# Kernel optimization log

Measured on AMD Instinct MI355X. Metric: run time of the kernel, lower is better.

Reference implementation:

```python
import jax, jax.numpy as jnp
import numpy as np

N_NODES = 50000
N_EDGES = 500000
N_FEAT = 128
EMB_DIM = 1024
HIDDEN = 128
OUT_DIM = 10
VOCAB = 55049
N_GRAPHS = 64


def setup_inputs() -> dict:
    key = jax.random.key(0)
    ks = jax.random.split(key, 12)
    x = jax.random.normal(ks[0], (N_NODES, N_FEAT), dtype=jnp.float32)
    edge_weight = jax.random.uniform(ks[1], (N_EDGES,), dtype=jnp.float32)
    edge_index = jax.random.randint(ks[2], (2, N_EDGES), 0, N_NODES)
    batch = jnp.sort(jax.random.randint(ks[3], (N_NODES,), 0, N_GRAPHS))
    node_ids = jax.random.randint(ks[4], (N_NODES,), 0, VOCAB)
    emb_table = jax.random.normal(ks[5], (VOCAB, EMB_DIM), dtype=jnp.float32)
    d_in = N_FEAT + EMB_DIM
    W1 = jax.random.normal(ks[6], (d_in, HIDDEN), dtype=jnp.float32) / np.sqrt(d_in)
    b1 = jnp.zeros((HIDDEN,), dtype=jnp.float32)
    W2 = jax.random.normal(ks[7], (HIDDEN, HIDDEN), dtype=jnp.float32) / np.sqrt(HIDDEN)
    b2 = jnp.zeros((HIDDEN,), dtype=jnp.float32)
    fcW = jax.random.normal(ks[8], (HIDDEN, OUT_DIM), dtype=jnp.float32) / np.sqrt(HIDDEN)
    fcb = jnp.zeros((OUT_DIM,), dtype=jnp.float32)
    return dict(x=x, edge_weight=edge_weight, emb_table=emb_table, W1=W1, b1=b1,
                W2=W2, b2=b2, fcW=fcW, fcb=fcb,
                edge_index=edge_index, batch=batch, node_ids=node_ids)


def gcn_conv(x, edge_index, edge_weight, W, b, n_nodes):
    # PyG GCNConv: x' = D^{-1/2} (A + I) D^{-1/2} (x W) + b, self-loop weight = 1
    x = x @ W
    src, dst = edge_index[0], edge_index[1]
    loop = jnp.arange(n_nodes)
    src = jnp.concatenate([src, loop])
    dst = jnp.concatenate([dst, loop])
    ew = jnp.concatenate([edge_weight, jnp.ones((n_nodes,), x.dtype)])
    deg = jax.ops.segment_sum(ew, dst, num_segments=n_nodes)
    dinv = jnp.where(deg > 0, jax.lax.rsqrt(deg), 0.0)
    norm = dinv[src] * ew * dinv[dst]  # [E+N]
    msgs = norm[:, None] * x[src]      # [E+N, H] gather
    out = jax.ops.segment_sum(msgs, dst, num_segments=n_nodes)  # scatter-add
    return out + b


def reference(x, edge_weight, emb_table, W1, b1, W2, b2, fcW, fcb,
              edge_index, batch, node_ids):
    n = x.shape[0]
    h = jnp.concatenate([x, emb_table[node_ids]], axis=1)  # [N, F+E]
    h = jax.nn.relu(gcn_conv(h, edge_index, edge_weight, W1, b1, n))
    h = jax.nn.relu(gcn_conv(h, edge_index, edge_weight, W2, b2, n))
    # global mean pool per graph (dropout is identity in eval)
    sums = jax.ops.segment_sum(h, batch, num_segments=N_GRAPHS)
    counts = jax.ops.segment_sum(jnp.ones((n,), h.dtype), batch, num_segments=N_GRAPHS)
    pooled = sums / jnp.maximum(counts, 1.0)[:, None]
    return pooled @ fcW + fcb
```

## Files before the change

### kernel.cpp

```cpp
#include <hip/hip_runtime.h>
#include <hip/hip_bf16.h>

#define N_NODES 50000
#define N_EDGES 500000
#define N_FEAT 128
#define EMB_DIM 1024
#define HIDDEN 128
#define OUT_DIM 10
#define N_GRAPHS 64
#define NB_NODE 196

typedef __attribute__((ext_vector_type(8))) short short8;
typedef __attribute__((ext_vector_type(4))) float f32x4;

__device__ __forceinline__ unsigned short f2bf(float f) {
    unsigned int u = __float_as_uint(f);
    return (unsigned short)((u + 0x7fffu + ((u >> 16) & 1u)) >> 16);
}
__device__ __forceinline__ float bflo(unsigned int r) { return __uint_as_float(r << 16); }
__device__ __forceinline__ float bfhi(unsigned int r) { return __uint_as_float(r & 0xffff0000u); }
__device__ __forceinline__ unsigned int packbf(float lo, float hi) {
    return ((unsigned int)f2bf(hi) << 16) | f2bf(lo);
}

__global__ __launch_bounds__(256) void k_init(unsigned long long* __restrict__ dc,
                                              float* __restrict__ sums,
                                              float* __restrict__ counts) {
    int i = blockIdx.x * 256 + threadIdx.x;
    if (i < N_NODES) dc[i] = 0ULL;
    if (i < N_GRAPHS * HIDDEN) sums[i] = 0.0f;
    if (i < N_GRAPHS) counts[i] = 0.0f;
}

__global__ __launch_bounds__(256) void k_deg(const int* __restrict__ dst,
                                             const float* __restrict__ ew,
                                             unsigned long long* __restrict__ dc) {
    int e = blockIdx.x * 256 + threadIdx.x;
    if (e < N_EDGES) {
        unsigned int fx = (unsigned int)(ew[e] * 16777216.0f);
        atomicAdd(&dc[dst[e]], (1ULL << 32) | (unsigned long long)fx);
    }
}

__global__ __launch_bounds__(256) void k_scan1(const unsigned long long* __restrict__ dc,
                                               int* __restrict__ bsum) {
    __shared__ int wsum[4];
    int i = blockIdx.x * 256 + threadIdx.x;
    int v = (i < N_NODES) ? (int)((const uint2*)dc)[i].y : 0;
#pragma unroll
    for (int off = 32; off; off >>= 1) v += __shfl_down(v, off, 64);
    if ((threadIdx.x & 63) == 0) wsum[threadIdx.x >> 6] = v;
    __syncthreads();
    if (threadIdx.x == 0) bsum[blockIdx.x] = wsum[0] + wsum[1] + wsum[2] + wsum[3];
}

__global__ __launch_bounds__(256) void k_scan2(int* __restrict__ bsum) {
    __shared__ int sh[256];
    int t = threadIdx.x;
    int v = (t < NB_NODE) ? bsum[t] : 0;
    sh[t] = v;
    __syncthreads();
    for (int off = 1; off < 256; off <<= 1) {
        int add = (t >= off) ? sh[t - off] : 0;
        __syncthreads();
        sh[t] += add;
        __syncthreads();
    }
    if (t < NB_NODE) bsum[t] = sh[t] - v;
}

__global__ __launch_bounds__(256) void k_scan3(const unsigned long long* __restrict__ dc,
                                               const int* __restrict__ bofs,
                                               int* __restrict__ cursor,
                                               int* __restrict__ rowptr,
                                               float* __restrict__ dinv) {
    __shared__ int sh[256];
    const int t = threadIdx.x;
    const int i = blockIdx.x * 256 + t;
    uint2 d = (i < N_NODES) ? ((const uint2*)dc)[i] : make_uint2(0u, 0u);
    int v = (int)d.y;
    sh[t] = v;
    __syncthreads();
    for (int off = 1; off < 256; off <<= 1) {
        int add = (t >= off) ? sh[t - off] : 0;
        __syncthreads();
        sh[t] += add;
        __syncthreads();
    }
    int ex = sh[t] - v + bofs[blockIdx.x];
    if (i < N_NODES) {
        rowptr[i] = ex;
        cursor[i] = ex;
        float deg = 1.0f + (float)d.x * (1.0f / 16777216.0f);
        dinv[i] = 1.0f / sqrtf(deg);
    }
    if (i == 0) rowptr[N_NODES] = N_EDGES;
}

__global__ __launch_bounds__(256) void k_fill(const int* __restrict__ src,
                                              const int* __restrict__ dst,
                                              const float* __restrict__ ew,
                                              const float* __restrict__ dinv,
                                              int* __restrict__ cursor,
                                              int2* __restrict__ csr) {
    int e = blockIdx.x * 256 + threadIdx.x;
    if (e >= N_EDGES) return;
    int s = src[e], d = dst[e];
    int pos = atomicAdd(&cursor[d], 1);
    float norm = dinv[s] * ew[e] * dinv[d];
    csr[pos] = make_int2(s, __float_as_int(norm));
}

__device__ __forceinline__ void prep_one(const float* __restrict__ W,
                                         unsigned short* __restrict__ Wt,
                                         int K, int t) {
    int n = t & 127;
    int c = t >> 7;
    if (c * 16 >= K) return;
    short8 h0, h1;
#pragma unroll
    for (int i = 0; i < 16; i++) {
        unsigned short h = f2bf(W[(size_t)(c * 16 + i) * HIDDEN + n]);
        if (i < 8) h0[i] = (short)h;
        else       h1[i - 8] = (short)h;
    }
    size_t o = (size_t)n * K + c * 16;
    *(short8*)&Wt[o] = h0;
    *(short8*)&Wt[o + 8] = h1;
}

__global__ __launch_bounds__(256) void k_prep(const float* __restrict__ W1,
                                              unsigned short* __restrict__ Wt1,
                                              const float* __restrict__ W2,
                                              unsigned short* __restrict__ Wt2) {
    int b = blockIdx.x;
    if (b < 36) prep_one(W1, Wt1, N_FEAT + EMB_DIM, b * 256 + threadIdx.x);
    else        prep_one(W2, Wt2, HIDDEN, (b - 36) * 256 + threadIdx.x);
}

template <int MODE>
__global__ __launch_bounds__(256) void k_gemm(const float* __restrict__ X,
                                              const unsigned short* __restrict__ Xb,
                                              const float* __restrict__ EMB,
                                              const int* __restrict__ ids,
                                              const unsigned short* __restrict__ Wt,
                                              unsigned short* __restrict__ tbf, int K) {
    __shared__ unsigned short As[128][40];
    __shared__ unsigned short Bs[128][40];

    const int tid = threadIdx.x;
    const int lane = tid & 63;
    const int wv = tid >> 6;
    const int wm = wv >> 1, wn = wv & 1;
    const int fr = lane & 15;
    const int fq = lane >> 4;
    const int mBase = blockIdx.x * 128;

    const int aRow = tid >> 1;
    const int aOff = (tid & 1) * 16;
    const int m = mBase + aRow;
    const int mc = (m < N_NODES) ? m : (N_NODES - 1);
    int embRow = 0;
    if (MODE == 0) embRow = ids[mc];

    f32x4 acc[4][4];
#pragma unroll
    for (int i = 0; i < 4; i++)
#pragma unroll
        for (int j = 0; j < 4; j++) acc[i][j] = (f32x4){0.f, 0.f, 0.f, 0.f};

    float av[16];
    short8 axb0, axb1;
    short8 bh0, bh1;
    {
        if (MODE == 0) {
            const float* aptr = X + (size_t)mc * N_FEAT + aOff;
            *(float4*)&av[0]  = *(const float4*)(aptr);
            *(float4*)&av[4]  = *(const float4*)(aptr + 4);
            *(float4*)&av[8]  = *(const float4*)(aptr + 8);
            *(float4*)&av[12] = *(const float4*)(aptr + 12);
        } else {
            const unsigned short* aptr = Xb + (size_t)mc * HIDDEN + aOff;
            axb0 = *(const short8*)(aptr);
            axb1 = *(const short8*)(aptr + 8);
        }
        size_t bo = (size_t)aRow * K + aOff;
        bh0 = *(const short8*)&Wt[bo];
        bh1 = *(const short8*)&Wt[bo + 8];
    }

    for (int k0 = 0; k0 < K; k0 += 32) {
        short8 ah0, ah1;
        if (MODE == 0) {
#pragma unroll
            for (int i = 0; i < 16; i++) {
                unsigned short h = f2bf(av[i]);
                if (i < 8) ah0[i] = (short)h;
                else       ah1[i - 8] = (short)h;
            }
        } else {
            ah0 = axb0; ah1 = axb1;
        }
        *(short8*)&As[aRow][aOff] = ah0; *(short8*)&As[aRow][aOff + 8] = ah1;
        *(short8*)&Bs[aRow][aOff] = bh0; *(short8*)&Bs[aRow][aOff + 8] = bh1;
        __syncthreads();

        int k1 = k0 + 32;
        if (k1 < K) {
            if (MODE == 0) {
                const float* aptr = (k1 < N_FEAT)
                    ? X + (size_t)mc * N_FEAT + k1 + aOff
                    : EMB + (size_t)embRow * EMB_DIM + (k1 - N_FEAT) + aOff;
                *(float4*)&av[0]  = *(const float4*)(aptr);
                *(float4*)&av[4]  = *(const float4*)(aptr + 4);
                *(float4*)&av[8]  = *(const float4*)(aptr + 8);
                *(float4*)&av[12] = *(const float4*)(aptr + 12);
            } else {
                const unsigned short* aptr = Xb + (size_t)mc * HIDDEN + k1 + aOff;
                axb0 = *(const short8*)(aptr);
                axb1 = *(const short8*)(aptr + 8);
            }
            size_t bo = (size_t)aRow * K + k1 + aOff;
            bh0 = *(const short8*)&Wt[bo];
            bh1 = *(const short8*)&Wt[bo + 8];
        }

        short8 aF[4], bF[4];
#pragma unroll
        for (int i = 0; i < 4; i++) {
            aF[i] = *(const short8*)&As[wm * 64 + i * 16 + fr][fq * 8];
            bF[i] = *(const short8*)&Bs[wn * 64 + i * 16 + fr][fq * 8];
        }

#pragma unroll
        for (int i = 0; i < 4; i++)
#pragma unroll
            for (int j = 0; j < 4; j++)
                acc[i][j] = __builtin_amdgcn_mfma_f32_16x16x32_bf16(aF[i], bF[j], acc[i][j], 0, 0, 0);
        __syncthreads();
    }

#pragma unroll
    for (int i = 0; i < 4; i++) {
#pragma unroll
        for (int j = 0; j < 4; j++) {
            int gcol = wn * 64 + j * 16 + fr;
#pragma unroll
            for (int r = 0; r < 4; r++) {
                int grow = mBase + wm * 64 + i * 16 + fq * 4 + r;
                if (grow < N_NODES) tbf[(size_t)grow * HIDDEN + gcol] = f2bf(acc[i][j][r]);
            }
        }
    }
}

template <int POOL, int NWAVE>
__global__ __launch_bounds__(NWAVE * 64) void k_agg(const int2* __restrict__ csr,
                                                    const int* __restrict__ rowptr,
                                                    const float* __restrict__ dinv,
                                                    const unsigned short* __restrict__ tbf,
                                                    const float* __restrict__ bias,
                                                    const int* __restrict__ batch,
                                                    unsigned short* __restrict__ outb,
                                                    float* __restrict__ sums,
                                                    float* __restrict__ counts) {
    __shared__ float lsum[HIDDEN];
    __shared__ int lcnt;
    const int wv = threadIdx.x >> 6;
    const int lane = threadIdx.x & 63;
    const int grp = lane >> 4;
    const int q = lane & 15;
    const int n = blockIdx.x * NWAVE + wv;
    const uint4* t128 = (const uint4*)tbf;

    if (POOL) {
        if (threadIdx.x < HIDDEN) lsum[threadIdx.x] = 0.f;
        if (threadIdx.x == 0) lcnt = 0;
        __syncthreads();
    }

    float acc[8] = {};
    if (n < N_NODES) {
        const int beg = rowptr[n];
        const int end = rowptr[n + 1];
        const float di = dinv[n];
        const float wself = (grp == 0) ? di * di : 0.f;
        uint4 sr = t128[(size_t)n * 16 + q];
        acc[0] = wself * bflo(sr.x); acc[1] = wself * bfhi(sr.x);
        acc[2] = wself * bflo(sr.y); acc[3] = wself * bfhi(sr.y);
        acc[4] = wself * bflo(sr.z); acc[5] = wself * bfhi(sr.z);
        acc[6] = wself * bflo(sr.w); acc[7] = wself * bfhi(sr.w);
        if (grp == 0) {
            float4 b0 = ((const float4*)bias)[q * 2];
            float4 b1 = ((const float4*)bias)[q * 2 + 1];
            acc[0] += b0.x; acc[1] += b0.y; acc[2] += b0.z; acc[3] += b0.w;
            acc[4] += b1.x; acc[5] += b1.y; acc[6] += b1.z; acc[7] += b1.w;
        }

        for (int base = beg; base < end; base += 64) {
            int cnt = end - base; if (cnt > 64) cnt = 64;
            int2 ce = (lane < cnt) ? csr[base + lane] : make_int2(0, 0);
            int j = 0;
            for (; j + 8 <= cnt; j += 8) {
                int   sA = __shfl(ce.x, j + grp);
                float wA = __int_as_float(__shfl(ce.y, j + grp));
                int   sB = __shfl(ce.x, j + 4 + grp);
                float wB = __int_as_float(__shfl(ce.y, j + 4 + grp));
                uint4 rA = t128[(size_t)sA * 16 + q];
                uint4 rB = t128[(size_t)sB * 16 + q];
                acc[0] = fmaf(wA, bflo(rA.x), acc[0]); acc[1] = fmaf(wA, bfhi(rA.x), acc[1]);
                acc[2] = fmaf(wA, bflo(rA.y), acc[2]); acc[3] = fmaf(wA, bfhi(rA.y), acc[3]);
                acc[4] = fmaf(wA, bflo(rA.z), acc[4]); acc[5] = fmaf(wA, bfhi(rA.z), acc[5]);
                acc[6] = fmaf(wA, bflo(rA.w), acc[6]); acc[7] = fmaf(wA, bfhi(rA.w), acc[7]);
                acc[0] = fmaf(wB, bflo(rB.x), acc[0]); acc[1] = fmaf(wB, bfhi(rB.x), acc[1]);
                acc[2] = fmaf(wB, bflo(rB.y), acc[2]); acc[3] = fmaf(wB, bfhi(rB.y), acc[3]);
                acc[4] = fmaf(wB, bflo(rB.z), acc[4]); acc[5] = fmaf(wB, bfhi(rB.z), acc[5]);
                acc[6] = fmaf(wB, bflo(rB.w), acc[6]); acc[7] = fmaf(wB, bfhi(rB.w), acc[7]);
            }
            for (; j < cnt; j += 4) {
                int   s = __shfl(ce.x, j + grp);
                float w = __int_as_float(__shfl(ce.y, j + grp));
                uint4 r = t128[(size_t)s * 16 + q];
                acc[0] = fmaf(w, bflo(r.x), acc[0]); acc[1] = fmaf(w, bfhi(r.x), acc[1]);
                acc[2] = fmaf(w, bflo(r.y), acc[2]); acc[3] = fmaf(w, bfhi(r.y), acc[3]);
                acc[4] = fmaf(w, bflo(r.z), acc[4]); acc[5] = fmaf(w, bfhi(r.z), acc[5]);
                acc[6] = fmaf(w, bflo(r.w), acc[6]); acc[7] = fmaf(w, bfhi(r.w), acc[7]);
            }
        }
    }

#pragma unroll
    for (int i = 0; i < 8; i++) {
        acc[i] += __shfl_xor(acc[i], 16);
        acc[i] += __shfl_xor(acc[i], 32);
    }

    if (!POOL) {
        if (n < N_NODES && grp == 0) {
#pragma unroll
            for (int i = 0; i < 8; i++) acc[i] = fmaxf(acc[i], 0.f);
            uint4 o;
            o.x = packbf(acc[0], acc[1]);
            o.y = packbf(acc[2], acc[3]);
            o.z = packbf(acc[4], acc[5]);
            o.w = packbf(acc[6], acc[7]);
            ((uint4*)outb)[(size_t)n * 16 + q] = o;
        }
    } else {
        if (n < N_NODES && grp == 0) {
#pragma unroll
            for (int i = 0; i < 8; i++) acc[i] = fmaxf(acc[i], 0.f);
            int g = batch[n];
            int g0 = batch[blockIdx.x * NWAVE];
            if (g == g0) {
#pragma unroll
                for (int i = 0; i < 8; i++) atomicAdd(&lsum[q * 8 + i], acc[i]);
                if (lane == 0) atomicAdd(&lcnt, 1);
            } else {
#pragma unroll
                for (int i = 0; i < 8; i++) atomicAdd(&sums[g * HIDDEN + q * 8 + i], acc[i]);
                if (lane == 0) atomicAdd(&counts[g], 1.0f);
            }
        }
        __syncthreads();
        int g0 = batch[blockIdx.x * NWAVE];
        if (threadIdx.x < HIDDEN) atomicAdd(&sums[g0 * HIDDEN + threadIdx.x], lsum[threadIdx.x]);
        if (threadIdx.x == 0) atomicAdd(&counts[g0], (float)lcnt);
    }
}

__global__ __launch_bounds__(64) void k_final(const float* __restrict__ sums,
                                              const float* __restrict__ counts,
                                              const float* __restrict__ fcW,
                                              const float* __restrict__ fcb,
                                              float* __restrict__ out) {
    int g = blockIdx.x;
    int o = threadIdx.x;
    if (o >= OUT_DIM) return;
    float inv = 1.0f / fmaxf(counts[g], 1.0f);
    float acc = 0.f;
    for (int f = 0; f < HIDDEN; f++)
        acc = fmaf(sums[g * HIDDEN + f], fcW[f * OUT_DIM + o], acc);
    out[g * OUT_DIM + o] = acc * inv + fcb[o];
}

extern "C" void kernel_launch(void* const* d_in, const int* in_sizes, int n_in,
                              void* d_out, int out_size, void* d_ws, size_t ws_size,
                              hipStream_t stream) {
    const float* x      = (const float*)d_in[0];
    const float* ew     = (const float*)d_in[1];
    const float* emb    = (const float*)d_in[2];
    const float* W1     = (const float*)d_in[3];
    const float* b1     = (const float*)d_in[4];
    const float* W2     = (const float*)d_in[5];
    const float* b2     = (const float*)d_in[6];
    const float* fcW    = (const float*)d_in[7];
    const float* fcb    = (const float*)d_in[8];
    const int* edge_idx = (const int*)d_in[9];
    const int* batch    = (const int*)d_in[10];
    const int* node_ids = (const int*)d_in[11];
    float* out = (float*)d_out;

    const int* src = edge_idx;
    const int* dst = edge_idx + N_EDGES;

    float* ws     = (float*)d_ws;
    float* dinv   = ws;
    unsigned long long* dc = (unsigned long long*)(ws + 50048);
    int*   cursor = (int*)(ws + 150048);
    int*   rowptr = (int*)(ws + 200096);
    int*   bsum   = (int*)(ws + 250152);
    int2*  csr    = (int2*)(ws + 250408);
    unsigned short* tbf   = (unsigned short*)(ws + 1250408);
    unsigned short* out1b = (unsigned short*)(ws + 4450408);
    float* sums   = ws + 7650408;
    float* counts = sums + N_GRAPHS * HIDDEN;
    unsigned short* wt1 = (unsigned short*)(ws + 7658664);
    unsigned short* wt2 = (unsigned short*)(ws + 7732392);

    const int NB_EDGE = (N_EDGES + 255) / 256;
    const int NB_GEMM = (N_NODES + 127) / 128;
    const int K1 = N_FEAT + EMB_DIM;

    k_init <<<NB_NODE, 256, 0, stream>>>(dc, sums, counts);
    k_deg  <<<NB_EDGE, 256, 0, stream>>>(dst, ew, dc);
    k_scan1<<<NB_NODE, 256, 0, stream>>>(dc, bsum);
    k_scan2<<<1, 256, 0, stream>>>(bsum);
    k_scan3<<<NB_NODE, 256, 0, stream>>>(dc, bsum, cursor, rowptr, dinv);
    k_fill <<<NB_EDGE, 256, 0, stream>>>(src, dst, ew, dinv, cursor, csr);
    k_prep <<<40, 256, 0, stream>>>(W1, wt1, W2, wt2);

    k_gemm<0><<<NB_GEMM, 256, 0, stream>>>(x, nullptr, emb, node_ids, wt1, tbf, K1);
    k_agg<0, 4><<<(N_NODES + 3) / 4, 256, 0, stream>>>(csr, rowptr, dinv, tbf, b1,
                                                       batch, out1b, sums, counts);

    k_gemm<1><<<NB_GEMM, 256, 0, stream>>>(nullptr, out1b, nullptr, nullptr, wt2, tbf, HIDDEN);
    k_agg<1, 16><<<(N_NODES + 15) / 16, 1024, 0, stream>>>(csr, rowptr, dinv, tbf, b2,
                                                           batch, nullptr, sums, counts);

    k_final<<<N_GRAPHS, 64, 0, stream>>>(sums, counts, fcW, fcb, out);
}
```

Measured before the change: 522.8 us.

## Fuse prep/scan launches, vectorize edge kernels, shrink GEMM tile, one node per quarter-wave

Folds the weight-prep kernel into the init kernel and merges the single-block scan into scan3, which cuts two launches. The edge degree and fill kernels now process four edges per thread using vector loads. The GEMM M-tile shrinks from 128 to 64 rows so more blocks are launched. The aggregation kernels give each 16-lane group its own node instead of splitting one node's edges across the wave, which removes the cross-group shuffle reduction but can leave lanes idle on nodes with uneven degree. Each scan3 block now redoes the full block-offset scan.

After: 548.8 us. 5.0% more time.

```diff
diff --git a/kernel.cpp b/kernel.cpp
--- a/kernel.cpp
+++ b/kernel.cpp
@@ -23,22 +23,55 @@
     return ((unsigned int)f2bf(hi) << 16) | f2bf(lo);
 }
 
+__device__ __forceinline__ void prep_one(const float* __restrict__ W,
+                                         unsigned short* __restrict__ Wt,
+                                         int K, int t) {
+    int n = t & 127;
+    int c = t >> 7;
+    if (c * 16 >= K) return;
+    short8 h0, h1;
+#pragma unroll
+    for (int i = 0; i < 16; i++) {
+        unsigned short h = f2bf(W[(size_t)(c * 16 + i) * HIDDEN + n]);
+        if (i < 8) h0[i] = (short)h;
+        else       h1[i - 8] = (short)h;
+    }
+    size_t o = (size_t)n * K + c * 16;
+    *(short8*)&Wt[o] = h0;
+    *(short8*)&Wt[o + 8] = h1;
+}
+
 __global__ __launch_bounds__(256) void k_init(unsigned long long* __restrict__ dc,
                                               float* __restrict__ sums,
-                                              float* __restrict__ counts) {
-    int i = blockIdx.x * 256 + threadIdx.x;
-    if (i < N_NODES) dc[i] = 0ULL;
-    if (i < N_GRAPHS * HIDDEN) sums[i] = 0.0f;
-    if (i < N_GRAPHS) counts[i] = 0.0f;
+                                              float* __restrict__ counts,
+                                              const float* __restrict__ W1,
+                                              unsigned short* __restrict__ Wt1,
+                                              const float* __restrict__ W2,
+                                              unsigned short* __restrict__ Wt2) {
+    int b = blockIdx.x;
+    if (b < NB_NODE) {
+        int i = b * 256 + threadIdx.x;
+        if (i < N_NODES) dc[i] = 0ULL;
+        if (i < N_GRAPHS * HIDDEN) sums[i] = 0.0f;
+        if (i < N_GRAPHS) counts[i] = 0.0f;
+    } else if (b < NB_NODE + 36) {
+        prep_one(W1, Wt1, N_FEAT + EMB_DIM, (b - NB_NODE) * 256 + threadIdx.x);
+    } else {
+        prep_one(W2, Wt2, HIDDEN, (b - NB_NODE - 36) * 256 + threadIdx.x);
+    }
 }
 
 __global__ __launch_bounds__(256) void k_deg(const int* __restrict__ dst,
                                              const float* __restrict__ ew,
                                              unsigned long long* __restrict__ dc) {
-    int e = blockIdx.x * 256 + threadIdx.x;
-    if (e < N_EDGES) {
-        unsigned int fx = (unsigned int)(ew[e] * 16777216.0f);
-        atomicAdd(&dc[dst[e]], (1ULL << 32) | (unsigned long long)fx);
+    int e4 = blockIdx.x * 256 + threadIdx.x;
+    if (e4 < N_EDGES / 4) {
+        int4 d4 = ((const int4*)dst)[e4];
+        float4 w4 = ((const float4*)ew)[e4];
+        atomicAdd(&dc[d4.x], (1ULL << 32) | (unsigned long long)(unsigned int)(w4.x * 16777216.0f));
+        atomicAdd(&dc[d4.y], (1ULL << 32) | (unsigned long long)(unsigned int)(w4.y * 16777216.0f));
+        atomicAdd(&dc[d4.z], (1ULL << 32) | (unsigned long long)(unsigned int)(w4.z * 16777216.0f));
+        atomicAdd(&dc[d4.w], (1ULL << 32) | (unsigned long long)(unsigned int)(w4.w * 16777216.0f));
     }
 }
 
@@ -54,28 +87,27 @@
     if (threadIdx.x == 0) bsum[blockIdx.x] = wsum[0] + wsum[1] + wsum[2] + wsum[3];
 }
 
-__global__ __launch_bounds__(256) void k_scan2(int* __restrict__ bsum) {
-    __shared__ int sh[256];
-    int t = threadIdx.x;
-    int v = (t < NB_NODE) ? bsum[t] : 0;
-    sh[t] = v;
-    __syncthreads();
-    for (int off = 1; off < 256; off <<= 1) {
-        int add = (t >= off) ? sh[t - off] : 0;
-        __syncthreads();
-        sh[t] += add;
-        __syncthreads();
-    }
-    if (t < NB_NODE) bsum[t] = sh[t] - v;
-}
-
 __global__ __launch_bounds__(256) void k_scan3(const unsigned long long* __restrict__ dc,
-                                               const int* __restrict__ bofs,
+                                               const int* __restrict__ bsum,
                                                int* __restrict__ cursor,
                                                int* __restrict__ rowptr,
                                                float* __restrict__ dinv) {
+    __shared__ int sb[256];
     __shared__ int sh[256];
+    __shared__ int bofs_s;
     const int t = threadIdx.x;
+
+    int vb = (t < NB_NODE) ? bsum[t] : 0;
+    sb[t] = vb;
+    __syncthreads();
+    for (int off = 1; off < 256; off <<= 1) {
+        int add = (t >= off) ? sb[t - off] : 0;
+        __syncthreads();
+        sb[t] += add;
+        __syncthreads();
+    }
+    if (t == blockIdx.x) bofs_s = sb[t] - vb;
+
     const int i = blockIdx.x * 256 + t;
     uint2 d = (i < N_NODES) ? ((const uint2*)dc)[i] : make_uint2(0u, 0u);
     int v = (int)d.y;
@@ -87,7 +119,7 @@
         sh[t] += add;
         __syncthreads();
     }
-    int ex = sh[t] - v + bofs[blockIdx.x];
+    int ex = sh[t] - v + bofs_s;
     if (i < N_NODES) {
         rowptr[i] = ex;
         cursor[i] = ex;
@@ -103,39 +135,27 @@
                                               const float* __restrict__ dinv,
                                               int* __restrict__ cursor,
                                               int2* __restrict__ csr) {
-    int e = blockIdx.x * 256 + threadIdx.x;
-    if (e >= N_EDGES) return;
-    int s = src[e], d = dst[e];
-    int pos = atomicAdd(&cursor[d], 1);
-    float norm = dinv[s] * ew[e] * dinv[d];
-    csr[pos] = make_int2(s, __float_as_int(norm));
-}
-
-__device__ __forceinline__ void prep_one(const float* __restrict__ W,
-                                         unsigned short* __restrict__ Wt,
-                                         int K, int t) {
-    int n = t & 127;
-    int c = t >> 7;
-    if (c * 16 >= K) return;
-    short8 h0, h1;
-#pragma unroll
-    for (int i = 0; i < 16; i++) {
-        unsigned short h = f2bf(W[(size_t)(c * 16 + i) * HIDDEN + n]);
-        if (i < 8) h0[i] = (short)h;
-        else       h1[i - 8] = (short)h;
-    }
-    size_t o = (size_t)n * K + c * 16;
-    *(short8*)&Wt[o] = h0;
-    *(short8*)&Wt[o + 8] = h1;
-}
-
-__global__ __launch_bounds__(256) void k_prep(const float* __restrict__ W1,
-                                              unsigned short* __restrict__ Wt1,
-                                              const float* __restrict__ W2,
-                                              unsigned short* __restrict__ Wt2) {
-    int b = blockIdx.x;
-    if (b < 36) prep_one(W1, Wt1, N_FEAT + EMB_DIM, b * 256 + threadIdx.x);
-    else        prep_one(W2, Wt2, HIDDEN, (b - 36) * 256 + threadIdx.x);
+    int e4 = blockIdx.x * 256 + threadIdx.x;
+    if (e4 >= N_EDGES / 4) return;
+    int4 s4 = ((const int4*)src)[e4];
+    int4 d4 = ((const int4*)dst)[e4];
+    float4 w4 = ((const float4*)ew)[e4];
+    {
+        int pos = atomicAdd(&cursor[d4.x], 1);
+        csr[pos] = make_int2(s4.x, __float_as_int(dinv[s4.x] * w4.x * dinv[d4.x]));
+    }
+    {
+        int pos = atomicAdd(&cursor[d4.y], 1);
+        csr[pos] = make_int2(s4.y, __float_as_int(dinv[s4.y] * w4.y * dinv[d4.y]));
+    }
+    {
+        int pos = atomicAdd(&cursor[d4.z], 1);
+        csr[pos] = make_int2(s4.z, __float_as_int(dinv[s4.z] * w4.z * dinv[d4.z]));
+    }
+    {
+        int pos = atomicAdd(&cursor[d4.w], 1);
+        csr[pos] = make_int2(s4.w, __float_as_int(dinv[s4.w] * w4.w * dinv[d4.w]));
+    }
 }
 
 template <int MODE>
@@ -145,7 +165,7 @@
                                               const int* __restrict__ ids,
                                               const unsigned short* __restrict__ Wt,
                                               unsigned short* __restrict__ tbf, int K) {
-    __shared__ unsigned short As[128][40];
+    __shared__ unsigned short As[64][40];
     __shared__ unsigned short Bs[128][40];
 
     const int tid = threadIdx.x;
@@ -154,55 +174,51 @@
     const int wm = wv >> 1, wn = wv & 1;
     const int fr = lane & 15;
     const int fq = lane >> 4;
-    const int mBase = blockIdx.x * 128;
-
-    const int aRow = tid >> 1;
-    const int aOff = (tid & 1) * 16;
+    const int mBase = blockIdx.x * 64;
+
+    const int aRow = tid >> 2;
+    const int aOff = (tid & 3) * 8;
+    const int bCol = tid >> 1;
+    const int bOff = (tid & 1) * 16;
+
     const int m = mBase + aRow;
     const int mc = (m < N_NODES) ? m : (N_NODES - 1);
     int embRow = 0;
     if (MODE == 0) embRow = ids[mc];
 
-    f32x4 acc[4][4];
-#pragma unroll
-    for (int i = 0; i < 4; i++)
+    f32x4 acc[2][4];
+#pragma unroll
+    for (int i = 0; i < 2; i++)
 #pragma unroll
         for (int j = 0; j < 4; j++) acc[i][j] = (f32x4){0.f, 0.f, 0.f, 0.f};
 
-    float av[16];
-    short8 axb0, axb1;
+    float av[8];
+    short8 axb;
     short8 bh0, bh1;
     {
         if (MODE == 0) {
             const float* aptr = X + (size_t)mc * N_FEAT + aOff;
-            *(float4*)&av[0]  = *(const float4*)(aptr);
-            *(float4*)&av[4]  = *(const float4*)(aptr + 4);
-            *(float4*)&av[8]  = *(const float4*)(aptr + 8);
-            *(float4*)&av[12] = *(const float4*)(aptr + 12);
+            *(float4*)&av[0] = *(const float4*)(aptr);
+            *(float4*)&av[4] = *(const float4*)(aptr + 4);
         } else {
-            const unsigned short* aptr = Xb + (size_t)mc * HIDDEN + aOff;
-            axb0 = *(const short8*)(aptr);
-            axb1 = *(const short8*)(aptr + 8);
-        }
-        size_t bo = (size_t)aRow * K + aOff;
+            axb = *(const short8*)(Xb + (size_t)mc * HIDDEN + aOff);
+        }
+        size_t bo = (size_t)bCol * K + bOff;
         bh0 = *(const short8*)&Wt[bo];
         bh1 = *(const short8*)&Wt[bo + 8];
     }
 
     for (int k0 = 0; k0 < K; k0 += 32) {
-        short8 ah0, ah1;
+        short8 ah;
         if (MODE == 0) {
 #pragma unroll
-            for (int i = 0; i < 16; i++) {
-                unsigned short h = f2bf(av[i]);
-                if (i < 8) ah0[i] = (short)h;
-                else       ah1[i - 8] = (short)h;
-            }
+            for (int i = 0; i < 8; i++) ah[i] = (short)f2bf(av[i]);
         } else {
-            ah0 = axb0; ah1 = axb1;
-        }
-        *(short8*)&As[aRow][aOff] = ah0; *(short8*)&As[aRow][aOff + 8] = ah1;
-        *(short8*)&Bs[aRow][aOff] = bh0; *(short8*)&Bs[aRow][aOff + 8] = bh1;
+            ah = axb;
+        }
+        *(short8*)&As[aRow][aOff] = ah;
+        *(short8*)&Bs[bCol][bOff] = bh0;
+        *(short8*)&Bs[bCol][bOff + 8] = bh1;
         __syncthreads();
 
         int k1 = k0 + 32;
@@ -211,29 +227,26 @@
                 const float* aptr = (k1 < N_FEAT)
                     ? X + (size_t)mc * N_FEAT + k1 + aOff
                     : EMB + (size_t)embRow * EMB_DIM + (k1 - N_FEAT) + aOff;
-                *(float4*)&av[0]  = *(const float4*)(aptr);
-                *(float4*)&av[4]  = *(const float4*)(aptr + 4);
-                *(float4*)&av[8]  = *(const float4*)(aptr + 8);
-                *(float4*)&av[12] = *(const float4*)(aptr + 12);
+                *(float4*)&av[0] = *(const float4*)(aptr);
+                *(float4*)&av[4] = *(const float4*)(aptr + 4);
             } else {
-                const unsigned short* aptr = Xb + (size_t)mc * HIDDEN + k1 + aOff;
-                axb0 = *(const short8*)(aptr);
-                axb1 = *(const short8*)(aptr + 8);
+                axb = *(const short8*)(Xb + (size_t)mc * HIDDEN + k1 + aOff);
             }
-            size_t bo = (size_t)aRow * K + k1 + aOff;
+            size_t bo = (size_t)bCol * K + k1 + bOff;
             bh0 = *(const short8*)&Wt[bo];
             bh1 = *(const short8*)&Wt[bo + 8];
         }
 
-        short8 aF[4], bF[4];
-#pragma unroll
-        for (int i = 0; i < 4; i++) {
-            aF[i] = *(const short8*)&As[wm * 64 + i * 16 + fr][fq * 8];
-            bF[i] = *(const short8*)&Bs[wn * 64 + i * 16 + fr][fq * 8];
-        }
-
-#pragma unroll
-        for (int i = 0; i < 4; i++)
+        short8 aF[2], bF[4];
+#pragma unroll
+        for (int i = 0; i < 2; i++)
+            aF[i] = *(const short8*)&As[wm * 32 + i * 16 + fr][fq * 8];
+#pragma unroll
+        for (int j = 0; j < 4; j++)
+            bF[j] = *(const short8*)&Bs[wn * 64 + j * 16 + fr][fq * 8];
+
+#pragma unroll
+        for (int i = 0; i < 2; i++)
 #pragma unroll
             for (int j = 0; j < 4; j++)
                 acc[i][j] = __builtin_amdgcn_mfma_f32_16x16x32_bf16(aF[i], bF[j], acc[i][j], 0, 0, 0);
@@ -241,13 +254,13 @@
     }
 
 #pragma unroll
-    for (int i = 0; i < 4; i++) {
+    for (int i = 0; i < 2; i++) {
 #pragma unroll
         for (int j = 0; j < 4; j++) {
             int gcol = wn * 64 + j * 16 + fr;
 #pragma unroll
             for (int r = 0; r < 4; r++) {
-                int grow = mBase + wm * 64 + i * 16 + fq * 4 + r;
+                int grow = mBase + wm * 32 + i * 16 + fq * 4 + r;
                 if (grow < N_NODES) tbf[(size_t)grow * HIDDEN + gcol] = f2bf(acc[i][j][r]);
             }
         }
@@ -268,9 +281,9 @@
     __shared__ int lcnt;
     const int wv = threadIdx.x >> 6;
     const int lane = threadIdx.x & 63;
-    const int grp = lane >> 4;
+    const int g = lane >> 4;
     const int q = lane & 15;
-    const int n = blockIdx.x * NWAVE + wv;
+    const int n = (blockIdx.x * NWAVE + wv) * 4 + g;
     const uint4* t128 = (const uint4*)tbf;
 
     if (POOL) {
@@ -284,61 +297,55 @@
         const int beg = rowptr[n];
         const int end = rowptr[n + 1];
         const float di = dinv[n];
-        const float wself = (grp == 0) ? di * di : 0.f;
+        const float wself = di * di;
         uint4 sr = t128[(size_t)n * 16 + q];
-        acc[0] = wself * bflo(sr.x); acc[1] = wself * bfhi(sr.x);
-        acc[2] = wself * bflo(sr.y); acc[3] = wself * bfhi(sr.y);
-        acc[4] = wself * bflo(sr.z); acc[5] = wself * bfhi(sr.z);
-        acc[6] = wself * bflo(sr.w); acc[7] = wself * bfhi(sr.w);
-        if (grp == 0) {
-            float4 b0 = ((const float4*)bias)[q * 2];
-            float4 b1 = ((const float4*)bias)[q * 2 + 1];
-            acc[0] += b0.x; acc[1] += b0.y; acc[2] += b0.z; acc[3] += b0.w;
-            acc[4] += b1.x; acc[5] += b1.y; acc[6] += b1.z; acc[7] += b1.w;
-        }
-
-        for (int base = beg; base < end; base += 64) {
-            int cnt = end - base; if (cnt > 64) cnt = 64;
-            int2 ce = (lane < cnt) ? csr[base + lane] : make_int2(0, 0);
-            int j = 0;
-            for (; j + 8 <= cnt; j += 8) {
-                int   sA = __shfl(ce.x, j + grp);
-                float wA = __int_as_float(__shfl(ce.y, j + grp));
-                int   sB = __shfl(ce.x, j + 4 + grp);
-                float wB = __int_as_float(__shfl(ce.y, j + 4 + grp));
-                uint4 rA = t128[(size_t)sA * 16 + q];
-                uint4 rB = t128[(size_t)sB * 16 + q];
-                acc[0] = fmaf(wA, bflo(rA.x), acc[0]); acc[1] = fmaf(wA, bfhi(rA.x), acc[1]);
-                acc[2] = fmaf(wA, bflo(rA.y), acc[2]); acc[3] = fmaf(wA, bfhi(rA.y), acc[3]);
-                acc[4] = fmaf(wA, bflo(rA.z), acc[4]); acc[5] = fmaf(wA, bfhi(rA.z), acc[5]);
-                acc[6] = fmaf(wA, bflo(rA.w), acc[6]); acc[7] = fmaf(wA, bfhi(rA.w), acc[7]);
-                acc[0] = fmaf(wB, bflo(rB.x), acc[0]); acc[1] = fmaf(wB, bfhi(rB.x), acc[1]);
-                acc[2] = fmaf(wB, bflo(rB.y), acc[2]); acc[3] = fmaf(wB, bfhi(rB.y), acc[3]);
-                acc[4] = fmaf(wB, bflo(rB.z), acc[4]); acc[5] = fmaf(wB, bfhi(rB.z), acc[5]);
-                acc[6] = fmaf(wB, bflo(rB.w), acc[6]); acc[7] = fmaf(wB, bfhi(rB.w), acc[7]);
+        float4 b0 = ((const float4*)bias)[q * 2];
+        float4 b1 = ((const float4*)bias)[q * 2 + 1];
+        acc[0] = fmaf(wself, bflo(sr.x), b0.x); acc[1] = fmaf(wself, bfhi(sr.x), b0.y);
+        acc[2] = fmaf(wself, bflo(sr.y), b0.z); acc[3] = fmaf(wself, bfhi(sr.y), b0.w);
+        acc[4] = fmaf(wself, bflo(sr.z), b1.x); acc[5] = fmaf(wself, bfhi(sr.z), b1.y);
+        acc[6] = fmaf(wself, bflo(sr.w), b1.z); acc[7] = fmaf(wself, bfhi(sr.w), b1.w);
+
+        for (int base = beg; base < end; base += 16) {
+            int cnt = end - base; if (cnt > 16) cnt = 16;
+            int2 ce = (q < cnt) ? csr[base + q] : make_int2(0, 0);
+            int rounds = (cnt + 3) >> 2;
+            for (int rr = 0; rr < rounds; rr++) {
+                int j0 = g * 16 + rr * 4;
+                int   s0 = __shfl(ce.x, j0),     s1 = __shfl(ce.x, j0 + 1);
+                int   s2 = __shfl(ce.x, j0 + 2), s3 = __shfl(ce.x, j0 + 3);
+                float w0 = __int_as_float(__shfl(ce.y, j0));
+                float w1 = __int_as_float(__shfl(ce.y, j0 + 1));
+                float w2 = __int_as_float(__shfl(ce.y, j0 + 2));
+                float w3 = __int_as_float(__shfl(ce.y, j0 + 3));
+                uint4 r0 = t128[(size_t)s0 * 16 + q];
+                uint4 r1 = t128[(size_t)s1 * 16 + q];
+                uint4 r2 = t128[(size_t)s2 * 16 + q];
+                uint4 r3 = t128[(size_t)s3 * 16 + q];
+                acc[0] = fmaf(w0, bflo(r0.x), acc[0]); acc[1] = fmaf(w0, bfhi(r0.x), acc[1]);
+                acc[2] = fmaf(w0, bflo(r0.y), acc[2]); acc[3] = fmaf(w0, bfhi(r0.y), acc[3]);
+                acc[4] = fmaf(w0, bflo(r0.z), acc[4]); acc[5] = fmaf(w0, bfhi(r0.z), acc[5]);
+                acc[6] = fmaf(w0, bflo(r0.w), acc[6]); acc[7] = fmaf(w0, bfhi(r0.w), acc[7]);
+                acc[0] = fmaf(w1, bflo(r1.x), acc[0]); acc[1] = fmaf(w1, bfhi(r1.x), acc[1]);
+                acc[2] = fmaf(w1, bflo(r1.y), acc[2]); acc[3] = fmaf(w1, bfhi(r1.y), acc[3]);
+                acc[4] = fmaf(w1, bflo(r1.z), acc[4]); acc[5] = fmaf(w1, bfhi(r1.z), acc[5]);
+                acc[6] = fmaf(w1, bflo(r1.w), acc[6]); acc[7] = fmaf(w1, bfhi(r1.w), acc[7]);
+                acc[0] = fmaf(w2, bflo(r2.x), acc[0]); acc[1] = fmaf(w2, bfhi(r2.x), acc[1]);
+                acc[2] = fmaf(w2, bflo(r2.y), acc[2]); acc[3] = fmaf(w2, bfhi(r2.y), acc[3]);
+                acc[4] = fmaf(w2, bflo(r2.z), acc[4]); acc[5] = fmaf(w2, bfhi(r2.z), acc[5]);
+                acc[6] = fmaf(w2, bflo(r2.w), acc[6]); acc[7] = fmaf(w2, bfhi(r2.w), acc[7]);
+                acc[0] = fmaf(w3, bflo(r3.x), acc[0]); acc[1] = fmaf(w3, bfhi(r3.x), acc[1]);
+                acc[2] = fmaf(w3, bflo(r3.y), acc[2]); acc[3] = fmaf(w3, bfhi(r3.y), acc[3]);
+                acc[4] = fmaf(w3, bflo(r3.z), acc[4]); acc[5] = fmaf(w3, bfhi(r3.z), acc[5]);
+                acc[6] = fmaf(w3, bflo(r3.w), acc[6]); acc[7] = fmaf(w3, bfhi(r3.w), acc[7]);
             }
-            for (; j < cnt; j += 4) {
-                int   s = __shfl(ce.x, j + grp);
-                float w = __int_as_float(__shfl(ce.y, j + grp));
-                uint4 r = t128[(size_t)s * 16 + q];
-                acc[0] = fmaf(w, bflo(r.x), acc[0]); acc[1] = fmaf(w, bfhi(r.x), acc[1]);
-                acc[2] = fmaf(w, bflo(r.y), acc[2]); acc[3] = fmaf(w, bfhi(r.y), acc[3]);
-                acc[4] = fmaf(w, bflo(r.z), acc[4]); acc[5] = fmaf(w, bfhi(r.z), acc[5]);
-                acc[6] = fmaf(w, bflo(r.w), acc[6]); acc[7] = fmaf(w, bfhi(r.w), acc[7]);
-            }
-        }
-    }
-
-#pragma unroll
-    for (int i = 0; i < 8; i++) {
-        acc[i] += __shfl_xor(acc[i], 16);
-        acc[i] += __shfl_xor(acc[i], 32);
+        }
+#pragma unroll
+        for (int i = 0; i < 8; i++) acc[i] = fmaxf(acc[i], 0.f);
     }
 
     if (!POOL) {
-        if (n < N_NODES && grp == 0) {
-#pragma unroll
-            for (int i = 0; i < 8; i++) acc[i] = fmaxf(acc[i], 0.f);
+        if (n < N_NODES) {
             uint4 o;
             o.x = packbf(acc[0], acc[1]);
             o.y = packbf(acc[2], acc[3]);
@@ -347,23 +354,21 @@
             ((uint4*)outb)[(size_t)n * 16 + q] = o;
         }
     } else {
-        if (n < N_NODES && grp == 0) {
-#pragma unroll
-            for (int i = 0; i < 8; i++) acc[i] = fmaxf(acc[i], 0.f);
-            int g = batch[n];
-            int g0 = batch[blockIdx.x * NWAVE];
-            if (g == g0) {
+        if (n < N_NODES) {
+            int gn = batch[n];
+            int g0 = batch[blockIdx.x * NWAVE * 4];
+            if (gn == g0) {
 #pragma unroll
                 for (int i = 0; i < 8; i++) atomicAdd(&lsum[q * 8 + i], acc[i]);
-                if (lane == 0) atomicAdd(&lcnt, 1);
+                if (q == 0) atomicAdd(&lcnt, 1);
             } else {
 #pragma unroll
-                for (int i = 0; i < 8; i++) atomicAdd(&sums[g * HIDDEN + q * 8 + i], acc[i]);
-                if (lane == 0) atomicAdd(&counts[g], 1.0f);
+                for (int i = 0; i < 8; i++) atomicAdd(&sums[gn * HIDDEN + q * 8 + i], acc[i]);
+                if (q == 0) atomicAdd(&counts[gn], 1.0f);
             }
         }
         __syncthreads();
-        int g0 = batch[blockIdx.x * NWAVE];
+        int g0 = batch[blockIdx.x * NWAVE * 4];
         if (threadIdx.x < HIDDEN) atomicAdd(&sums[g0 * HIDDEN + threadIdx.x], lsum[threadIdx.x]);
         if (threadIdx.x == 0) atomicAdd(&counts[g0], (float)lcnt);
     }
@@ -418,24 +423,22 @@
     unsigned short* wt1 = (unsigned short*)(ws + 7658664);
     unsigned short* wt2 = (unsigned short*)(ws + 7732392);
 
-    const int NB_EDGE = (N_EDGES + 255) / 256;
-    const int NB_GEMM = (N_NODES + 127) / 128;
+    const int NB_EDGE4 = (N_EDGES / 4 + 255) / 256;
+    const int NB_GEMM  = (N_NODES + 63) / 64;
     const int K1 = N_FEAT + EMB_DIM;
 
-    k_init <<<NB_NODE, 256, 0, stream>>>(dc, sums, counts);
-    k_deg  <<<NB_EDGE, 256, 0, stream>>>(dst, ew, dc);
+    k_init <<<NB_NODE + 40, 256, 0, stream>>>(dc, sums, counts, W1, wt1, W2, wt2);
+    k_deg  <<<NB_EDGE4, 256, 0, stream>>>(dst, ew, dc);
     k_scan1<<<NB_NODE, 256, 0, stream>>>(dc, bsum);
-    k_scan2<<<1, 256, 0, stream>>>(bsum);
     k_scan3<<<NB_NODE, 256, 0, stream>>>(dc, bsum, cursor, rowptr, dinv);
-    k_fill <<<NB_EDGE, 256, 0, stream>>>(src, dst, ew, dinv, cursor, csr);
-    k_prep <<<40, 256, 0, stream>>>(W1, wt1, W2, wt2);
+    k_fill <<<NB_EDGE4, 256, 0, stream>>>(src, dst, ew, dinv, cursor, csr);
 
     k_gemm<0><<<NB_GEMM, 256, 0, stream>>>(x, nullptr, emb, node_ids, wt1, tbf, K1);
-    k_agg<0, 4><<<(N_NODES + 3) / 4, 256, 0, stream>>>(csr, rowptr, dinv, tbf, b1,
-                                                       batch, out1b, sums, counts);
+    k_agg<0, 4><<<(N_NODES + 15) / 16, 256, 0, stream>>>(csr, rowptr, dinv, tbf, b1,
+                                                         batch, out1b, sums, counts);
 
     k_gemm<1><<<NB_GEMM, 256, 0, stream>>>(nullptr, out1b, nullptr, nullptr, wt2, tbf, HIDDEN);
-    k_agg<1, 16><<<(N_NODES + 15) / 16, 1024, 0, stream>>>(csr, rowptr, dinv, tbf, b2,
+    k_agg<1, 16><<<(N_NODES + 63) / 64, 1024, 0, stream>>>(csr, rowptr, dinv, tbf, b2,
                                                            batch, nullptr, sums, counts);
 
     k_final<<<N_GRAPHS, 64, 0, stream>>>(sums, counts, fcW, fcb, out);
```
